# Optimization experiments

Hardware: AMD Instinct MI355X
Metric: run time of the kernel (lower is better)

The kernel has to match this reference:

```python
import jax, jax.numpy as jnp
import numpy as np

T, H, E, K, I = 8192, 1024, 8, 2, 512  # tokens, hidden, experts, top_k, expert_intermediate
IS = I * 1  # shared-expert intermediate = expert_intermediate_size * num_shared_experts


def setup_inputs() -> dict:
    key = jax.random.key(0)
    ks = jax.random.split(key, 6)
    s = lambda *d: 1.0 / np.sqrt(d[0])
    return {
        "hidden_states": jax.random.normal(ks[0], (T, H), dtype=jnp.float32),
        "w_gate": jax.random.normal(ks[1], (H, E), dtype=jnp.float32) * s(H),
        "w_experts_gate_up": jax.random.normal(ks[2], (E, H, 2 * I), dtype=jnp.float32) * s(H),
        "w_experts_down": jax.random.normal(ks[3], (E, I, H), dtype=jnp.float32) * s(I),
        "w_shared_gate_up": jax.random.normal(ks[4], (H, 2 * IS), dtype=jnp.float32) * s(H),
        "w_shared_down": jax.random.normal(ks[5], (IS, H), dtype=jnp.float32) * s(IS),
    }


def _silu_and_mul(gu):
    d = gu.shape[-1] // 2
    return jax.nn.silu(gu[..., :d]) * gu[..., d:]


def reference(hidden_states, w_gate, w_experts_gate_up, w_experts_down,
              w_shared_gate_up, w_shared_down):
    x = hidden_states  # [T, H]

    # shared expert: SwiGLU MLP (reduce_results=False path)
    shared_out = _silu_and_mul(x @ w_shared_gate_up) @ w_shared_down  # [T, H]

    # router gate + top-k with renormalization (norm_expert_prob=True)
    router_logits = x @ w_gate  # [T, E]
    probs = jax.nn.softmax(router_logits.astype(jnp.float32), axis=-1)
    topk_w, topk_idx = jax.lax.top_k(probs, K)  # [T, K]
    topk_w = topk_w / jnp.sum(topk_w, axis=-1, keepdims=True)
    # scatter top-k weights into a sparse [T, E] combine matrix
    full_w = jnp.zeros((T, E), dtype=x.dtype)
    full_w = full_w.at[jnp.arange(T)[:, None], topk_idx].set(topk_w.astype(x.dtype))

    # expert SwiGLU MLPs (grouped GEMM expressed as batched einsum over experts)
    gu = jnp.einsum('th,ehi->eti', x, w_experts_gate_up)       # [E, T, 2I]
    act = _silu_and_mul(gu)                                     # [E, T, I]
    expert_out = jnp.einsum('eti,eih->eth', act, w_experts_down)  # [E, T, H]

    # weighted combine over selected experts (weights are zero elsewhere)
    moe_out = jnp.einsum('te,eth->th', full_w, expert_out)     # [T, H]

    return moe_out + shared_out
```

## Files before the change

### kernel.cpp

```cpp
#include <hip/hip_runtime.h>
#include <hip/hip_bf16.h>
#include <cstdint>

#define T_TOK 8192
#define HID   1024
#define NE    9
#define ISZ   512
#define RBASE 18432
#define NSLOT (RBASE + T_TOK)

#define BM 256
#define NROWB (NSLOT / BM)

typedef unsigned short u16;
typedef unsigned int   u32;
typedef signed char    i8;
typedef __attribute__((ext_vector_type(8))) short short8;
typedef __attribute__((ext_vector_type(4))) float f32x4;
typedef __attribute__((ext_vector_type(4))) int   i32x4;

__device__ __forceinline__ u16 f2bf(float f) {
  u32 u = __builtin_bit_cast(u32, f);
  return (u16)((u + 0x7fffu + ((u >> 16) & 1u)) >> 16);
}
__device__ __forceinline__ float bf2f(u16 v) {
  return __builtin_bit_cast(float, (u32)v << 16);
}
__device__ __forceinline__ int q8(float v, float inv) {
  int q = (int)__builtin_rintf(v * inv);
  return (q > 127) ? 127 : ((q < -127) ? -127 : q);
}
__device__ __forceinline__ int colp_of(int c) {
  int i = (c < 512) ? c : (c - 512);
  return (i >> 4) * 32 + ((c < 512) ? 0 : 16) + (i & 15);
}

#define STAGE(gp, lp) __builtin_amdgcn_global_load_lds( \
    (__attribute__((address_space(1))) u32*)(gp),       \
    (__attribute__((address_space(3))) u32*)(lp), 16, 0, 0)

__global__ __launch_bounds__(256) void k_wamax_part(
    const float* __restrict__ wgu, const float* __restrict__ wsg,
    float* __restrict__ pmax) {
  const int e = blockIdx.y, hb = blockIdx.x;
  const float* src = (e < 8) ? (wgu + (size_t)e * 1048576) : wsg;
  const int wv = threadIdx.x >> 6, l = threadIdx.x & 63;
  float4 m4[4];
#pragma unroll
  for (int j = 0; j < 4; ++j) m4[j] = make_float4(0.f, 0.f, 0.f, 0.f);
  const int r0 = hb * 16 + wv * 4;
#pragma unroll
  for (int r = 0; r < 4; ++r) {
    const float* row = src + (size_t)(r0 + r) * 1024;
#pragma unroll
    for (int j = 0; j < 4; ++j) {
      const float4 v = *(const float4*)&row[j * 256 + l * 4];
      m4[j].x = fmaxf(m4[j].x, fabsf(v.x));
      m4[j].y = fmaxf(m4[j].y, fabsf(v.y));
      m4[j].z = fmaxf(m4[j].z, fabsf(v.z));
      m4[j].w = fmaxf(m4[j].w, fabsf(v.w));
    }
  }
  __shared__ float4 red[4][4][64];
#pragma unroll
  for (int j = 0; j < 4; ++j) red[wv][j][l] = m4[j];
  __syncthreads();
  const int j2 = threadIdx.x >> 6, l2 = threadIdx.x & 63;
  const float4 a = red[0][j2][l2], b = red[1][j2][l2];
  const float4 c = red[2][j2][l2], d = red[3][j2][l2];
  float4 o;
  o.x = fmaxf(fmaxf(a.x, b.x), fmaxf(c.x, d.x));
  o.y = fmaxf(fmaxf(a.y, b.y), fmaxf(c.y, d.y));
  o.z = fmaxf(fmaxf(a.z, b.z), fmaxf(c.z, d.z));
  o.w = fmaxf(fmaxf(a.w, b.w), fmaxf(c.w, d.w));
  *(float4*)&pmax[((size_t)e * 64 + hb) * 1024 + j2 * 256 + l2 * 4] = o;
}

__global__ __launch_bounds__(256) void k_wamax_red(
    const float* __restrict__ pmax, float* __restrict__ swc) {
  const int flat = blockIdx.x * 256 + threadIdx.x;
  const int e = flat >> 10, c = flat & 1023;
  float m = 0.f;
  for (int hb = 0; hb < 64; ++hb)
    m = fmaxf(m, pmax[((size_t)e * 64 + hb) * 1024 + c]);
  swc[e * 1024 + colp_of(c)] = m * (1.f / 127.f);
}

#define NB_WGUP (32 * 8 * NE)
#define NB_WDN  (32 * 4 * NE)
#define NB_RTR  (T_TOK / 4)

__global__ __launch_bounds__(256) void k_prep(
    const float* __restrict__ x, const float* __restrict__ wg,
    const float* __restrict__ wgu, const float* __restrict__ wsg,
    const float* __restrict__ wdn, const float* __restrict__ wsd,
    const float* __restrict__ swc,
    i8* __restrict__ xq, float* __restrict__ sxg,
    i8* __restrict__ wguq, u16* __restrict__ wdT,
    int* __restrict__ eidx, float2* __restrict__ wts) {
  __shared__ float tile[32][129];
  const int b = blockIdx.x;
  const int tid = threadIdx.x;

  if (b < NB_WGUP) {
    const int e = b / 256, rem = b % 256;
    const int c0 = (rem & 31) * 32, h0 = (rem >> 5) * 128;
    const float* src = (e < 8) ? (wgu + (size_t)e * HID * 1024) : wsg;
    const int hl = tid >> 1, cb = (tid & 1) * 16;
#pragma unroll
    for (int j = 0; j < 4; ++j) {
      const float4 v = *(const float4*)&src[(size_t)(h0 + hl) * 1024 + c0 + cb + j * 4];
      tile[cb + j * 4 + 0][hl] = v.x;
      tile[cb + j * 4 + 1][hl] = v.y;
      tile[cb + j * 4 + 2][hl] = v.z;
      tile[cb + j * 4 + 3][hl] = v.w;
    }
    __syncthreads();
    const int cl = tid >> 3, hb = (tid & 7) * 16;
    const int cp = colp_of(c0 + cl);
    const float inv = 1.f / swc[e * 1024 + cp];
    i8 out[16];
#pragma unroll
    for (int k = 0; k < 16; ++k) out[k] = (i8)q8(tile[cl][hb + k], inv);
    *(int4*)&wguq[((size_t)e * 1024 + cp) * 1024 + h0 + hb] = *(int4*)out;
    return;
  }
  if (b < NB_WGUP + NB_WDN) {
    const int bb = b - NB_WGUP;
    const int e = bb / 128, r2 = bb % 128;
    const int h0 = (r2 & 31) * 32, i0 = (r2 >> 5) * 128;
    const float* src = (e < 8) ? (wdn + (size_t)e * ISZ * HID) : wsd;
    const int il = tid >> 1, hb2 = (tid & 1) * 16;
#pragma unroll
    for (int j = 0; j < 4; ++j) {
      const float4 v = *(const float4*)&src[(size_t)(i0 + il) * 1024 + h0 + hb2 + j * 4];
      tile[hb2 + j * 4 + 0][il] = v.x;
      tile[hb2 + j * 4 + 1][il] = v.y;
      tile[hb2 + j * 4 + 2][il] = v.z;
      tile[hb2 + j * 4 + 3][il] = v.w;
    }
    __syncthreads();
    const int hl2 = tid >> 3, ib = (tid & 7) * 16;
    u16 ob[16];
#pragma unroll
    for (int k = 0; k < 16; ++k) ob[k] = f2bf(tile[hl2][ib + k]);
    u16* dst = &wdT[((size_t)e * HID + h0 + hl2) * ISZ + i0 + ib];
    *(int4*)dst = *(int4*)ob;
    *(int4*)(dst + 8) = *(int4*)(ob + 8);
    return;
  }
  const int t = (b - NB_WGUP - NB_WDN) * 4 + (tid >> 6);
  const int l = tid & 63;
  float a[8] = {0, 0, 0, 0, 0, 0, 0, 0};
  float vals[16];
  float am = 0.f;
  const float4* xr4 = (const float4*)(x + (size_t)t * HID);
#pragma unroll
  for (int j = 0; j < 4; ++j) {
    const float4 v = xr4[j * 64 + l];
    vals[4 * j] = v.x; vals[4 * j + 1] = v.y; vals[4 * j + 2] = v.z; vals[4 * j + 3] = v.w;
    am = fmaxf(am, fmaxf(fmaxf(fabsf(v.x), fabsf(v.y)), fmaxf(fabsf(v.z), fabsf(v.w))));
    const int h = (j * 64 + l) * 4;
#pragma unroll
    for (int i = 0; i < 4; ++i) {
      const float4 w0 = *(const float4*)&wg[(h + i) * 8];
      const float4 w1 = *(const float4*)&wg[(h + i) * 8 + 4];
      const float ev = vals[4 * j + i];
      a[0] += ev * w0.x; a[1] += ev * w0.y; a[2] += ev * w0.z; a[3] += ev * w0.w;
      a[4] += ev * w1.x; a[5] += ev * w1.y; a[6] += ev * w1.z; a[7] += ev * w1.w;
    }
  }
#pragma unroll
  for (int off = 32; off >= 1; off >>= 1) {
    am = fmaxf(am, __shfl_xor(am, off));
#pragma unroll
    for (int e2 = 0; e2 < 8; ++e2) a[e2] += __shfl_xor(a[e2], off);
  }
  const float inv = (am > 0.f) ? 127.f / am : 0.f;
  u32* xq4 = (u32*)(xq + (size_t)t * HID);
#pragma unroll
  for (int j = 0; j < 4; ++j) {
    u32 q = ((u32)(unsigned char)(i8)q8(vals[4 * j], inv)) |
            ((u32)(unsigned char)(i8)q8(vals[4 * j + 1], inv) << 8) |
            ((u32)(unsigned char)(i8)q8(vals[4 * j + 2], inv) << 16) |
            ((u32)(unsigned char)(i8)q8(vals[4 * j + 3], inv) << 24);
    xq4[j * 64 + l] = q;
  }
  if (l == 0) {
    sxg[t] = am * (1.f / 127.f);
    int ia = 0;
#pragma unroll
    for (int e2 = 1; e2 < 8; ++e2) if (a[e2] > a[ia]) ia = e2;
    int ib = (ia == 0) ? 1 : 0;
#pragma unroll
    for (int e2 = 0; e2 < 8; ++e2) if (e2 != ia && a[e2] > a[ib]) ib = e2;
    float wa = 1.f / (1.f + expf(a[ib] - a[ia]));
    eidx[t] = ia | (ib << 8);
    wts[t] = make_float2(wa, 1.f - wa);
  }
}

__global__ __launch_bounds__(512) void k_scatter(
    const int* __restrict__ eidx, int* __restrict__ btok, int* __restrict__ slotmap,
    int* __restrict__ seg, int* __restrict__ segcnt) {
  __shared__ int cnt_s[8];
  __shared__ int goff_s[9];
  const int e = threadIdx.x >> 6;
  const int l = threadIdx.x & 63;

  int c1 = 0;
  for (int c = 0; c < T_TOK / 64; ++c) {
    int v = eidx[c * 64 + l];
    c1 += __popcll(__ballot((v & 255) == e)) + __popcll(__ballot(((v >> 8) & 255) == e));
  }
  if (l == 0) cnt_s[e] = c1;
  __syncthreads();
  if (threadIdx.x == 0) {
    int off = 0;
    for (int k = 0; k < 8; ++k) { goff_s[k] = off; off += (cnt_s[k] + 255) & ~255; }
    goff_s[8] = off;
  }
  __syncthreads();
  const int base0 = goff_s[e];
  const int cnt_e = cnt_s[e];
  const unsigned long long below = (l == 63) ? ~0ull >> 1 : ((1ull << l) - 1);

  int base = base0;
  for (int c = 0; c < T_TOK / 64; ++c) {
    const int t = c * 64 + l;
    const int v = eidx[t];
    const unsigned long long ma = __ballot((v & 255) == e);
    const unsigned long long mb = __ballot(((v >> 8) & 255) == e);
    if ((v & 255) == e) {
      int s = base + __popcll(ma & below);
      btok[s] = t; slotmap[2 * t] = s;
    }
    if (((v >> 8) & 255) == e) {
      int s = base + __popcll(ma) + __popcll(mb & below);
      btok[s] = t; slotmap[2 * t + 1] = s;
    }
    base += __popcll(ma) + __popcll(mb);
  }
  for (int p = cnt_e + l; p < ((cnt_e + 255) & ~255); p += 64) btok[base0 + p] = 0;
  if (threadIdx.x < 9) seg[threadIdx.x] = goff_s[threadIdx.x];
  if (threadIdx.x < 8) segcnt[threadIdx.x] = cnt_s[threadIdx.x];
}

__device__ __forceinline__ bool seg_lookup(const int* __restrict__ seg,
                                           const int* __restrict__ segcnt,
                                           int brow, int& e) {
  if (brow >= RBASE) { e = 8; return true; }
  if (brow >= seg[8]) return false;
  e = 0;
#pragma unroll
  for (int k = 1; k < 8; ++k) if (brow >= seg[k]) e = k;
  return brow < seg[e] + segcnt[e];
}


#define G1_STG(kt) do {                                             \
    const int _ra = ((kt) % 3) * 32768;                             \
    STAGE(sA0 + (kt) * 128, Ab + _ra + 0 * 8192 + w * 1024);        \
    STAGE(sA1 + (kt) * 128, Ab + _ra + 1 * 8192 + w * 1024);        \
    STAGE(sA2 + (kt) * 128, Ab + _ra + 2 * 8192 + w * 1024);        \
    STAGE(sA3 + (kt) * 128, Ab + _ra + 3 * 8192 + w * 1024);        \
    const int _rb = ((kt) % 3) * 16384;                             \
    STAGE(sB0 + (kt) * 128, Bb + _rb + 0 * 8192 + w * 1024);        \
    STAGE(sB1 + (kt) * 128, Bb + _rb + 1 * 8192 + w * 1024); } while (0)

#define G1_LOADF(SA, SB, RG, KX) do {                               \
    _Pragma("unroll") for (int m = 0; m < 4; ++m)                   \
      SA[m] = *(const i32x4*)&Ab[(RG) * 32768 + aBase + m * 2048 + (KX)]; \
    _Pragma("unroll") for (int n = 0; n < 4; ++n)                   \
      SB[n] = *(const i32x4*)&Bb[(RG) * 16384 + bBase + n * 2048 + (KX)]; } while (0)

#define G1_MFMA(SA, SB) do { __builtin_amdgcn_s_setprio(1);         \
    _Pragma("unroll") for (int m = 0; m < 4; ++m)                   \
      _Pragma("unroll") for (int n = 0; n < 4; ++n)                 \
        acc[m][n] = __builtin_amdgcn_mfma_i32_16x16x64_i8(SA[m], SB[n], acc[m][n], 0, 0, 0); \
    __builtin_amdgcn_s_setprio(0); } while (0)

__global__ __launch_bounds__(512) void k_gemm_gu(
    const i8* __restrict__ xq,
    const i8* __restrict__ wguq,
    const int* __restrict__ seg, const int* __restrict__ segcnt,
    const int* __restrict__ btok, const float* __restrict__ sxg,
    const float* __restrict__ swc,
    u16* __restrict__ act)
{
  const int bid = blockIdx.x;
  const int brow = (bid % NROWB) * BM;
  const int bcol = (bid / NROWB) * 128;
  int e;
  if (!seg_lookup(seg, segcnt, brow, e)) return;

  __shared__ __align__(16) i8 Ab[3 * 32768];
  __shared__ __align__(16) i8 Bb[3 * 16384];
  __shared__ float sxl[BM];
  __shared__ float swcl[128];

  const int tid = threadIdx.x;
  const int w = tid >> 6, l = tid & 63;
  const int wm = w >> 1, wn = w & 1;
  const int fr = l & 15, fg = l >> 4;

  if (tid < BM) {
    const int rrow = brow + tid;
    const int tk = (e < 8) ? btok[rrow] : (rrow - RBASE);
    sxl[tid] = sxg[tk];
  }
  if (tid >= BM && tid < BM + 128) swcl[tid - BM] = swc[e * 1024 + bcol + (tid - BM)];

  const int rr = w * 8 + (l >> 3);
  const int sw = ((l & 7) ^ (l >> 3)) * 16;
  int tr[4];
#pragma unroll
  for (int j = 0; j < 4; ++j) {
    const int gr = brow + j * 64 + rr;
    tr[j] = (e < 8) ? btok[gr] : (gr - RBASE);
  }
  const i8* sA0 = xq + (size_t)tr[0] * HID + sw;
  const i8* sA1 = xq + (size_t)tr[1] * HID + sw;
  const i8* sA2 = xq + (size_t)tr[2] * HID + sw;
  const i8* sA3 = xq + (size_t)tr[3] * HID + sw;
  const i8* sB0 = wguq + ((size_t)e * 1024 + bcol + 0 * 64 + rr) * HID + sw;
  const i8* sB1 = wguq + ((size_t)e * 1024 + bcol + 1 * 64 + rr) * HID + sw;

  const int aBase = (wm * 64 + fr) * 128;
  const int bBase = (wn * 64 + fr) * 128;
  const int kx0 = (fg ^ (fr & 7)) * 16;
  const int kx1 = kx0 ^ 64;

  i32x4 acc[4][4];
#pragma unroll
  for (int m = 0; m < 4; ++m)
#pragma unroll
    for (int n = 0; n < 4; ++n) acc[m][n] = (i32x4){0, 0, 0, 0};
  i32x4 fA0[4], fB0[4], fA1[4], fB1[4];

  const int NKT = HID / 128;
  G1_STG(0); G1_STG(1);
  asm volatile("s_waitcnt vmcnt(6)" ::: "memory");
  __builtin_amdgcn_s_barrier();
  for (int s = 0; s < NKT; ++s) {
    const int rg = s % 3;
    if (s + 2 < NKT) G1_STG(s + 2);
    G1_LOADF(fA0, fB0, rg, kx0);
    __builtin_amdgcn_sched_barrier(0);
    G1_LOADF(fA1, fB1, rg, kx1);
    asm volatile("s_waitcnt lgkmcnt(8)" ::: "memory");
    __builtin_amdgcn_sched_barrier(0);
    G1_MFMA(fA0, fB0);
    asm volatile("s_waitcnt lgkmcnt(0)" ::: "memory");
    __builtin_amdgcn_sched_barrier(0);
    G1_MFMA(fA1, fB1);
    if (s + 1 < NKT) {
      if (s + 2 < NKT) { asm volatile("s_waitcnt vmcnt(6)" ::: "memory"); }
      else             { asm volatile("s_waitcnt vmcnt(0)" ::: "memory"); }
      __builtin_amdgcn_s_barrier();
    }
  }

#pragma unroll
  for (int m = 0; m < 4; ++m) {
#pragma unroll
    for (int p = 0; p < 2; ++p) {
      const i32x4 gI = acc[m][2 * p], uI = acc[m][2 * p + 1];
      const int col = ((bcol + wn * 64) >> 1) + p * 16 + fr;
      const float swg = swcl[wn * 64 + p * 32 + fr];
      const float swu = swcl[wn * 64 + p * 32 + 16 + fr];
#pragma unroll
      for (int r = 0; r < 4; ++r) {
        const int row_l = wm * 64 + m * 16 + fg * 4 + r;
        const float sx = sxl[row_l];
        const float gate = (float)gI[r] * (sx * swg);
        const float up   = (float)uI[r] * (sx * swu);
        const float sv = gate / (1.f + __expf(-gate));
        act[(size_t)(brow + row_l) * ISZ + col] = f2bf(sv * up);
      }
    }
  }
}


#define D_STGA(kt) do { const int _d = ((kt) % 3) * 8192 + w * 1024; \
    STAGE(dA0 + (kt) * 32, As + _d);                                 \
    STAGE(dA1 + (kt) * 32, As + _d + 512); } while (0)
#define D_STGB(kt) do { const int _d = ((kt) % 3) * 8192 + w * 1024; \
    STAGE(dB0 + (kt) * 32, Bs + _d);                                 \
    STAGE(dB1 + (kt) * 32, Bs + _d + 512); } while (0)
#define D_LDA4(sl, mb) do {                                          \
    af[0] = *(const short8*)&As[(sl) + aOff + ((mb) + 0) * 512];     \
    af[1] = *(const short8*)&As[(sl) + aOff + ((mb) + 1) * 512];     \
    af[2] = *(const short8*)&As[(sl) + aOff + ((mb) + 2) * 512];     \
    af[3] = *(const short8*)&As[(sl) + aOff + ((mb) + 3) * 512]; } while (0)
#define D_LDB4(sl) do {                                              \
    bf[0] = *(const short8*)&Bs[(sl) + bOff + 0 * 512];              \
    bf[1] = *(const short8*)&Bs[(sl) + bOff + 1 * 512];              \
    bf[2] = *(const short8*)&Bs[(sl) + bOff + 2 * 512];              \
    bf[3] = *(const short8*)&Bs[(sl) + bOff + 3 * 512]; } while (0)
#define D_MFMA16(mb) do { __builtin_amdgcn_s_setprio(1);             \
    _Pragma("unroll") for (int mm = 0; mm < 4; ++mm)                 \
      _Pragma("unroll") for (int nn = 0; nn < 4; ++nn)               \
        accf[(mb) + mm][nn] = __builtin_amdgcn_mfma_f32_16x16x32_bf16( \
            af[mm], bf[nn], accf[(mb) + mm][nn], 0, 0, 0);           \
    __builtin_amdgcn_s_setprio(0); } while (0)

__global__ __launch_bounds__(512) void k_gemm_down(
    const u16* __restrict__ act, const u16* __restrict__ wdT,
    const int* __restrict__ seg, const int* __restrict__ segcnt,
    u16* __restrict__ tmp) {
  const int brow = blockIdx.x * BM;
  const int bcol = blockIdx.y * 256;
  int e;
  if (!seg_lookup(seg, segcnt, brow, e)) return;

  __shared__ __align__(16) u16 As[3 * 8192];
  __shared__ __align__(16) u16 Bs[3 * 8192];

  const int tid = threadIdx.x;
  const int w = tid >> 6, l = tid & 63;
  const int wm = w >> 2, wn = w & 3;
  const int fr = l & 15, fg = l >> 4;

  const int arow0 = (w * 128 + l) >> 2;
  const int swd = ((l & 3) ^ (arow0 & 3)) * 8;
  const u16* dA0 = act + (size_t)(brow + arow0) * ISZ + swd;
  const u16* dA1 = act + (size_t)(brow + arow0 + 16) * ISZ + swd;
  const u16* dB0 = wdT + ((size_t)e * 1024 + bcol + arow0) * ISZ + swd;
  const u16* dB1 = wdT + ((size_t)e * 1024 + bcol + arow0 + 16) * ISZ + swd;

  const int aOff = (wm * 128 + fr) * 32 + ((fg ^ (fr & 3)) * 8);
  const int bOff = (wn * 64 + fr) * 32 + ((fg ^ (fr & 3)) * 8);

  f32x4 accf[8][4];
#pragma unroll
  for (int m = 0; m < 8; ++m)
#pragma unroll
    for (int n = 0; n < 4; ++n) accf[m][n] = (f32x4){0.f, 0.f, 0.f, 0.f};
  short8 af[4], bf[4];

  const int NKT = ISZ / 32;
  D_STGA(0); D_STGB(0); D_STGA(1); D_STGB(1);
  asm volatile("s_waitcnt vmcnt(4)" ::: "memory");
  __builtin_amdgcn_s_barrier();
  for (int kt = 0; kt < NKT; ++kt) {
    const int sl = (kt % 3) * 8192;
    D_LDA4(sl, 0); D_LDB4(sl);
    if (kt + 2 < NKT) D_STGA(kt + 2);
    __builtin_amdgcn_s_barrier();
    asm volatile("s_waitcnt lgkmcnt(0)" ::: "memory");
    __builtin_amdgcn_sched_barrier(0);
    D_MFMA16(0);
    __builtin_amdgcn_s_barrier();
    D_LDA4(sl, 4);
    if (kt + 2 < NKT) D_STGB(kt + 2);
    __builtin_amdgcn_s_barrier();
    asm volatile("s_waitcnt lgkmcnt(0)" ::: "memory");
    __builtin_amdgcn_sched_barrier(0);
    D_MFMA16(4);
    if (kt + 2 < NKT)      { asm volatile("s_waitcnt vmcnt(4)" ::: "memory"); }
    else if (kt + 1 < NKT) { asm volatile("s_waitcnt vmcnt(0)" ::: "memory"); }
    __builtin_amdgcn_s_barrier();
  }

#pragma unroll
  for (int m = 0; m < 8; ++m) {
#pragma unroll
    for (int r = 0; r < 4; ++r) {
      const int row = brow + wm * 128 + m * 16 + fg * 4 + r;
#pragma unroll
      for (int n = 0; n < 4; ++n) {
        const int col = bcol + wn * 64 + n * 16 + fr;
        tmp[(size_t)row * HID + col] = f2bf(accf[m][n][r]);
      }
    }
  }
}

__global__ __launch_bounds__(256) void k_combine(
    const u16* __restrict__ tmp, const int* __restrict__ slotmap,
    const float2* __restrict__ wts, float* __restrict__ out) {
  const int idx = blockIdx.x * 256 + threadIdx.x;
  const int t = idx >> 7;
  const int c = (idx & 127) << 3;
  const int s0 = slotmap[2 * t], s1 = slotmap[2 * t + 1];
  const float2 wv = wts[t];
  const short8 a = *(const short8*)(tmp + (size_t)s0 * HID + c);
  const short8 b = *(const short8*)(tmp + (size_t)s1 * HID + c);
  const short8 s = *(const short8*)(tmp + (size_t)(RBASE + t) * HID + c);
  float r[8];
#pragma unroll
  for (int j = 0; j < 8; ++j)
    r[j] = bf2f((u16)s[j]) + wv.x * bf2f((u16)a[j]) + wv.y * bf2f((u16)b[j]);
  float* po = out + (size_t)t * HID + c;
  *(float4*)po       = make_float4(r[0], r[1], r[2], r[3]);
  *(float4*)(po + 4) = make_float4(r[4], r[5], r[6], r[7]);
}

extern "C" void kernel_launch(void* const* d_in, const int* in_sizes, int n_in,
                              void* d_out, int out_size, void* d_ws, size_t ws_size,
                              hipStream_t stream) {
  const float* x   = (const float*)d_in[0];
  const float* wg  = (const float*)d_in[1];
  const float* wgu = (const float*)d_in[2];
  const float* wdn = (const float*)d_in[3];
  const float* wsg = (const float*)d_in[4];
  const float* wsd = (const float*)d_in[5];
  float* out = (float*)d_out;

  char* ws = (char*)d_ws;
  i8*  xq    = (i8*)ws;   ws += (size_t)T_TOK * HID;
  i8*  wguq  = (i8*)ws;   ws += (size_t)NE * 1024 * HID;
  u16* wdT   = (u16*)ws;  ws += (size_t)NE * HID * ISZ * 2;
  u16* actb  = (u16*)ws;  ws += (size_t)NSLOT * ISZ * 2;
  u16* tmp   = (u16*)ws;  ws += (size_t)NSLOT * HID * 2;
  float* sxg = (float*)ws; ws += (size_t)T_TOK * 4;
  float* swc = (float*)ws; ws += (size_t)NE * 1024 * 4;
  float* pmx = (float*)ws; ws += (size_t)NE * 64 * 1024 * 4;
  int* eidx  = (int*)ws;  ws += (size_t)T_TOK * 4;
  float2* wt = (float2*)ws; ws += (size_t)T_TOK * 8;
  int* btok  = (int*)ws;  ws += (size_t)RBASE * 4;
  int* smap  = (int*)ws;  ws += (size_t)2 * T_TOK * 4;
  int* seg   = (int*)ws;  ws += 16 * 4;
  int* segc  = (int*)ws;

  k_wamax_part<<<dim3(64, NE), 256, 0, stream>>>(wgu, wsg, pmx);
  k_wamax_red<<<(NE * 1024) / 256, 256, 0, stream>>>(pmx, swc);
  k_prep<<<NB_WGUP + NB_WDN + NB_RTR, 256, 0, stream>>>(
      x, wg, wgu, wsg, wdn, wsd, swc, xq, sxg, wguq, wdT, eidx, wt);
  k_scatter<<<1, 512, 0, stream>>>(eidx, btok, smap, seg, segc);
  k_gemm_gu<<<NROWB * 8, 512, 0, stream>>>(
      xq, wguq, seg, segc, btok, sxg, swc, actb);
  k_gemm_down<<<dim3(NROWB, HID / 256), 512, 0, stream>>>(actb, wdT, seg, segc, tmp);
  k_combine<<<(T_TOK * HID / 8) / 256, 256, 0, stream>>>(tmp, smap, wt, out);
}
```

Before: 211.5 us.

## Widen gate-up GEMM tile to 256 columns with double-buffered LDS

The int8 gate/up GEMM block tile grows from 256x128 to 256x256, so each wave holds a 64x128 accumulator set (32 MFMA tiles) and half as many blocks are launched. The LDS pipeline drops from triple to double buffering so the larger B tile still fits, and fragment loads are now issued and consumed one K-half at a time instead of preloading both. This raises arithmetic intensity per A-tile load and halves redundant token-row gathers, at the cost of higher register pressure, fewer blocks for occupancy and load balance, and shallower prefetch with a full vmcnt(0) wait every step.

```diff
diff --git a/kernel.cpp b/kernel.cpp
--- a/kernel.cpp
+++ b/kernel.cpp
@@ -258,26 +258,26 @@
 }
 
 
-#define G1_STG(kt) do {                                             \
-    const int _ra = ((kt) % 3) * 32768;                             \
-    STAGE(sA0 + (kt) * 128, Ab + _ra + 0 * 8192 + w * 1024);        \
-    STAGE(sA1 + (kt) * 128, Ab + _ra + 1 * 8192 + w * 1024);        \
-    STAGE(sA2 + (kt) * 128, Ab + _ra + 2 * 8192 + w * 1024);        \
-    STAGE(sA3 + (kt) * 128, Ab + _ra + 3 * 8192 + w * 1024);        \
-    const int _rb = ((kt) % 3) * 16384;                             \
-    STAGE(sB0 + (kt) * 128, Bb + _rb + 0 * 8192 + w * 1024);        \
-    STAGE(sB1 + (kt) * 128, Bb + _rb + 1 * 8192 + w * 1024); } while (0)
-
-#define G1_LOADF(SA, SB, RG, KX) do {                               \
+#define G1_STG(kt) do { const int _r = ((kt) & 1) * 32768;          \
+    STAGE(sA0 + (kt) * 128, Ab + _r + 0 * 8192 + w * 1024);         \
+    STAGE(sA1 + (kt) * 128, Ab + _r + 1 * 8192 + w * 1024);         \
+    STAGE(sA2 + (kt) * 128, Ab + _r + 2 * 8192 + w * 1024);         \
+    STAGE(sA3 + (kt) * 128, Ab + _r + 3 * 8192 + w * 1024);         \
+    STAGE(sB0 + (kt) * 128, Bb + _r + 0 * 8192 + w * 1024);         \
+    STAGE(sB1 + (kt) * 128, Bb + _r + 1 * 8192 + w * 1024);         \
+    STAGE(sB2 + (kt) * 128, Bb + _r + 2 * 8192 + w * 1024);         \
+    STAGE(sB3 + (kt) * 128, Bb + _r + 3 * 8192 + w * 1024); } while (0)
+
+#define G1_LOADF(RG, KX) do {                                       \
     _Pragma("unroll") for (int m = 0; m < 4; ++m)                   \
-      SA[m] = *(const i32x4*)&Ab[(RG) * 32768 + aBase + m * 2048 + (KX)]; \
-    _Pragma("unroll") for (int n = 0; n < 4; ++n)                   \
-      SB[n] = *(const i32x4*)&Bb[(RG) * 16384 + bBase + n * 2048 + (KX)]; } while (0)
-
-#define G1_MFMA(SA, SB) do { __builtin_amdgcn_s_setprio(1);         \
+      fA[m] = *(const i32x4*)&Ab[(RG) * 32768 + aBase + m * 2048 + (KX)]; \
+    _Pragma("unroll") for (int n = 0; n < 8; ++n)                   \
+      fB[n] = *(const i32x4*)&Bb[(RG) * 32768 + bBase + n * 2048 + (KX)]; } while (0)
+
+#define G1_MFMA do { __builtin_amdgcn_s_setprio(1);                 \
     _Pragma("unroll") for (int m = 0; m < 4; ++m)                   \
-      _Pragma("unroll") for (int n = 0; n < 4; ++n)                 \
-        acc[m][n] = __builtin_amdgcn_mfma_i32_16x16x64_i8(SA[m], SB[n], acc[m][n], 0, 0, 0); \
+      _Pragma("unroll") for (int n = 0; n < 8; ++n)                 \
+        acc[m][n] = __builtin_amdgcn_mfma_i32_16x16x64_i8(fA[m], fB[n], acc[m][n], 0, 0, 0); \
     __builtin_amdgcn_s_setprio(0); } while (0)
 
 __global__ __launch_bounds__(512) void k_gemm_gu(
@@ -290,14 +290,14 @@
 {
   const int bid = blockIdx.x;
   const int brow = (bid % NROWB) * BM;
-  const int bcol = (bid / NROWB) * 128;
+  const int bcol = (bid / NROWB) * 256;
   int e;
   if (!seg_lookup(seg, segcnt, brow, e)) return;
 
-  __shared__ __align__(16) i8 Ab[3 * 32768];
-  __shared__ __align__(16) i8 Bb[3 * 16384];
+  __shared__ __align__(16) i8 Ab[2 * 32768];
+  __shared__ __align__(16) i8 Bb[2 * 32768];
   __shared__ float sxl[BM];
-  __shared__ float swcl[128];
+  __shared__ float swcl[256];
 
   const int tid = threadIdx.x;
   const int w = tid >> 6, l = tid & 63;
@@ -308,8 +308,9 @@
     const int rrow = brow + tid;
     const int tk = (e < 8) ? btok[rrow] : (rrow - RBASE);
     sxl[tid] = sxg[tk];
-  }
-  if (tid >= BM && tid < BM + 128) swcl[tid - BM] = swc[e * 1024 + bcol + (tid - BM)];
+  } else {
+    swcl[tid - 256] = swc[e * 1024 + bcol + (tid - 256)];
+  }
 
   const int rr = w * 8 + (l >> 3);
   const int sw = ((l & 7) ^ (l >> 3)) * 16;
@@ -325,50 +326,48 @@
   const i8* sA3 = xq + (size_t)tr[3] * HID + sw;
   const i8* sB0 = wguq + ((size_t)e * 1024 + bcol + 0 * 64 + rr) * HID + sw;
   const i8* sB1 = wguq + ((size_t)e * 1024 + bcol + 1 * 64 + rr) * HID + sw;
+  const i8* sB2 = wguq + ((size_t)e * 1024 + bcol + 2 * 64 + rr) * HID + sw;
+  const i8* sB3 = wguq + ((size_t)e * 1024 + bcol + 3 * 64 + rr) * HID + sw;
 
   const int aBase = (wm * 64 + fr) * 128;
-  const int bBase = (wn * 64 + fr) * 128;
+  const int bBase = (wn * 128 + fr) * 128;
   const int kx0 = (fg ^ (fr & 7)) * 16;
   const int kx1 = kx0 ^ 64;
 
-  i32x4 acc[4][4];
+  i32x4 acc[4][8];
 #pragma unroll
   for (int m = 0; m < 4; ++m)
 #pragma unroll
-    for (int n = 0; n < 4; ++n) acc[m][n] = (i32x4){0, 0, 0, 0};
-  i32x4 fA0[4], fB0[4], fA1[4], fB1[4];
+    for (int n = 0; n < 8; ++n) acc[m][n] = (i32x4){0, 0, 0, 0};
+  i32x4 fA[4], fB[8];
 
   const int NKT = HID / 128;
-  G1_STG(0); G1_STG(1);
-  asm volatile("s_waitcnt vmcnt(6)" ::: "memory");
+  G1_STG(0);
+  asm volatile("s_waitcnt vmcnt(0)" ::: "memory");
   __builtin_amdgcn_s_barrier();
   for (int s = 0; s < NKT; ++s) {
-    const int rg = s % 3;
-    if (s + 2 < NKT) G1_STG(s + 2);
-    G1_LOADF(fA0, fB0, rg, kx0);
-    __builtin_amdgcn_sched_barrier(0);
-    G1_LOADF(fA1, fB1, rg, kx1);
-    asm volatile("s_waitcnt lgkmcnt(8)" ::: "memory");
-    __builtin_amdgcn_sched_barrier(0);
-    G1_MFMA(fA0, fB0);
+    const int rg = s & 1;
+    if (s + 1 < NKT) G1_STG(s + 1);
+    G1_LOADF(rg, kx0);
     asm volatile("s_waitcnt lgkmcnt(0)" ::: "memory");
     __builtin_amdgcn_sched_barrier(0);
-    G1_MFMA(fA1, fB1);
-    if (s + 1 < NKT) {
-      if (s + 2 < NKT) { asm volatile("s_waitcnt vmcnt(6)" ::: "memory"); }
-      else             { asm volatile("s_waitcnt vmcnt(0)" ::: "memory"); }
-      __builtin_amdgcn_s_barrier();
-    }
+    G1_MFMA;
+    G1_LOADF(rg, kx1);
+    asm volatile("s_waitcnt lgkmcnt(0)" ::: "memory");
+    __builtin_amdgcn_sched_barrier(0);
+    G1_MFMA;
+    asm volatile("s_waitcnt vmcnt(0)" ::: "memory");
+    __builtin_amdgcn_s_barrier();
   }
 
 #pragma unroll
   for (int m = 0; m < 4; ++m) {
 #pragma unroll
-    for (int p = 0; p < 2; ++p) {
+    for (int p = 0; p < 4; ++p) {
       const i32x4 gI = acc[m][2 * p], uI = acc[m][2 * p + 1];
-      const int col = ((bcol + wn * 64) >> 1) + p * 16 + fr;
-      const float swg = swcl[wn * 64 + p * 32 + fr];
-      const float swu = swcl[wn * 64 + p * 32 + 16 + fr];
+      const int col = ((bcol + wn * 128) >> 1) + p * 16 + fr;
+      const float swg = swcl[wn * 128 + p * 32 + fr];
+      const float swu = swcl[wn * 128 + p * 32 + 16 + fr];
 #pragma unroll
       for (int r = 0; r < 4; ++r) {
         const int row_l = wm * 64 + m * 16 + fg * 4 + r;
@@ -530,7 +529,7 @@
   k_prep<<<NB_WGUP + NB_WDN + NB_RTR, 256, 0, stream>>>(
       x, wg, wgu, wsg, wdn, wsd, swc, xq, sxg, wguq, wdT, eidx, wt);
   k_scatter<<<1, 512, 0, stream>>>(eidx, btok, smap, seg, segc);
-  k_gemm_gu<<<NROWB * 8, 512, 0, stream>>>(
+  k_gemm_gu<<<NROWB * 4, 512, 0, stream>>>(
       xq, wguq, seg, segc, btok, sxg, swc, actb);
   k_gemm_down<<<dim3(NROWB, HID / 256), 512, 0, stream>>>(actb, wdT, seg, segc, tmp);
   k_combine<<<(T_TOK * HID / 8) / 256, 256, 0, stream>>>(tmp, smap, wt, out);
```

Result: faster. 206.3 us (-2.5%).
